# Kernel tuning notes

Measured on AMD Instinct MI355X. Metric: run time of the kernel, lower is better.

Reference implementation:

```python
import jax, jax.numpy as jnp
import numpy as np

D_MODEL, D_K, D_V, H = 1024, 64, 64, 16
B, NQ, NK = 2, 2048, 2048


def setup_inputs() -> dict:
    key = jax.random.key(0)
    ks = jax.random.split(key, 12)
    hd = H * D_K
    xav = lambda k, shape: jax.random.uniform(k, shape, jnp.float32, -1.0, 1.0) * np.sqrt(6.0 / (shape[0] + shape[1]))
    return {
        "queries": jax.random.normal(ks[0], (B, NQ, D_MODEL), jnp.float32),
        "keys": jax.random.normal(ks[1], (B, NK, D_MODEL), jnp.float32),
        "values": jax.random.normal(ks[2], (B, NK, D_MODEL), jnp.float32),
        "memory": jax.random.uniform(ks[3], (B, NK), jnp.float32),
        "Wq": xav(ks[4], (D_MODEL, hd)), "bq": jnp.zeros((hd,), jnp.float32),
        "Wk": xav(ks[5], (D_MODEL, hd)), "bk": jnp.zeros((hd,), jnp.float32),
        "Wv": xav(ks[6], (D_MODEL, H * D_V)), "bv": jnp.zeros((H * D_V,), jnp.float32),
        "Wo": xav(ks[7], (H * D_V, D_MODEL)), "bo": jnp.zeros((D_MODEL,), jnp.float32),
        "Wmm": xav(ks[8], (1, H * D_V)), "bmm": jnp.zeros((H * D_V,), jnp.float32),
    }


def reference(queries, keys, values, memory, Wq, bq, Wk, bk, Wv, bv, Wo, bo, Wmm, bmm):
    b, nq = queries.shape[:2]
    nk = keys.shape[1]
    # projections -> (b, h, n, d)
    q = (queries @ Wq + bq).reshape(b, nq, H, D_K).transpose(0, 2, 1, 3)
    k = (keys @ Wk + bk).reshape(b, nk, H, D_K).transpose(0, 2, 1, 3)
    v = (values @ Wv + bv).reshape(b, nk, H, D_V).transpose(0, 2, 1, 3)
    # memory gate: fc_mm(memory[..., None]) -> (b, nk, h*d_k) -> (b, h, nk, d_k)
    mm = (memory[:, :, None] * Wmm[0] + bmm).reshape(b, nk, H, D_K).transpose(0, 2, 1, 3)
    att = jnp.einsum("bhqd,bhkd->bhqk", q, k * mm) / np.sqrt(D_K).astype(np.float32)
    att = jax.nn.softmax(att, axis=-1)
    out = jnp.einsum("bhqk,bhkd->bhqd", att, v * mm)
    out = out.transpose(0, 2, 1, 3).reshape(b, nq, H * D_V)
    return out @ Wo + bo
```

## Files before the change

### kernel.cpp

```cpp
#include <hip/hip_runtime.h>
#include <hip/hip_bf16.h>

#define H_   16
#define NQ_  2048
#define NK_  2048
#define DM_  1024

typedef float f32x4 __attribute__((ext_vector_type(4)));
typedef __bf16 bf16x8 __attribute__((ext_vector_type(8)));
typedef unsigned short u16x8 __attribute__((ext_vector_type(8)));

__device__ __forceinline__ unsigned short bfbits(float x) {
  __bf16 h = (__bf16)x;
  return __builtin_bit_cast(unsigned short, h);
}

__global__ __launch_bounds__(256) void cvt3(const float* __restrict__ q,
                                            const float* __restrict__ k,
                                            const float* __restrict__ v,
                                            unsigned short* __restrict__ qo,
                                            unsigned short* __restrict__ ko,
                                            unsigned short* __restrict__ vo) {
  const float* src = (blockIdx.y == 0) ? q : (blockIdx.y == 1) ? k : v;
  unsigned short* dst = (blockIdx.y == 0) ? qo : (blockIdx.y == 1) ? ko : vo;
  int i = blockIdx.x * 256 + threadIdx.x;
  const float4* s4 = (const float4*)src;
  float4 a = s4[2 * i], b = s4[2 * i + 1];
  bf16x8 o;
  o[0] = (__bf16)a.x; o[1] = (__bf16)a.y; o[2] = (__bf16)a.z; o[3] = (__bf16)a.w;
  o[4] = (__bf16)b.x; o[5] = (__bf16)b.y; o[6] = (__bf16)b.z; o[7] = (__bf16)b.w;
  *((bf16x8*)dst + i) = o;
}

__global__ __launch_bounds__(256) void transpose_cvt4(
    const float* __restrict__ s0, const float* __restrict__ s1,
    const float* __restrict__ s2, const float* __restrict__ s3,
    unsigned short* __restrict__ d0, unsigned short* __restrict__ d1,
    unsigned short* __restrict__ d2, unsigned short* __restrict__ d3) {
  const float* src = (blockIdx.z == 0) ? s0 : (blockIdx.z == 1) ? s1 : (blockIdx.z == 2) ? s2 : s3;
  unsigned short* dst = (blockIdx.z == 0) ? d0 : (blockIdx.z == 1) ? d1 : (blockIdx.z == 2) ? d2 : d3;
  __shared__ float t[64][65];
  const int r0 = blockIdx.x * 64, c0 = blockIdx.y * 64;
  for (int i = threadIdx.x; i < 4096; i += 256) {
    int r = i >> 6, c = i & 63;
    t[r][c] = src[(size_t)(r0 + r) * DM_ + c0 + c];
  }
  __syncthreads();
  for (int i = threadIdx.x; i < 4096; i += 256) {
    int n = i >> 6, k = i & 63;
    dst[(size_t)(c0 + n) * DM_ + r0 + k] = bfbits(t[k][n]);
  }
}

__device__ __forceinline__ void gll16(const unsigned short* g, unsigned short* l) {
  __builtin_amdgcn_global_load_lds((const __attribute__((address_space(1))) void*)g,
                                   (__attribute__((address_space(3))) void*)l, 16, 0, 0);
}

template <int MODE>
__device__ __forceinline__ void gemm128_body(
    int bx, int by,
    const unsigned short* __restrict__ A, const unsigned short* __restrict__ Bt, int K,
    const float* __restrict__ bias, const float* __restrict__ mem,
    const float* __restrict__ Wmm, const float* __restrict__ bmm,
    unsigned short* __restrict__ obf,
    unsigned short* Al, unsigned short* Bl) {
  const int tid = threadIdx.x, lane = tid & 63, w = tid >> 6;
  const int wm = w >> 1, wn = w & 1;
  const int m0 = bx * 128, n0 = by * 128;
  const int lrow = lane >> 2, lcol = (lane & 3) * 8;
  const int fr = lane & 15, fk = (lane >> 4) * 8;

  f32x4 acc[4][4] = {};

  const unsigned short* ag0 = A + (size_t)(m0 + w * 32 + lrow) * K + lcol;
  const unsigned short* bg0 = Bt + (size_t)(n0 + w * 32 + lrow) * K + lcol;
  unsigned short* la0 = &Al[(w * 32) * 32];
  unsigned short* la1 = &Al[(w * 32 + 16) * 32];
  unsigned short* lb0 = &Bl[(w * 32) * 32];
  unsigned short* lb1 = &Bl[(w * 32 + 16) * 32];
  const size_t s16K = (size_t)16 * K;

  const int KT = K >> 5;
  for (int kt = 0; kt < KT; ++kt) {
    gll16(ag0, la0); gll16(ag0 + s16K, la1);
    gll16(bg0, lb0); gll16(bg0 + s16K, lb1);
    ag0 += 32; bg0 += 32;
    __syncthreads();
    bf16x8 af[4], bfr[4];
#pragma unroll
    for (int i = 0; i < 4; ++i) af[i] = *(const bf16x8*)&Al[(wm * 64 + i * 16 + fr) * 32 + fk];
#pragma unroll
    for (int j = 0; j < 4; ++j) bfr[j] = *(const bf16x8*)&Bl[(wn * 64 + j * 16 + fr) * 32 + fk];
#pragma unroll
    for (int i = 0; i < 4; ++i)
#pragma unroll
      for (int j = 0; j < 4; ++j)
        acc[i][j] = __builtin_amdgcn_mfma_f32_16x16x32_bf16(af[i], bfr[j], acc[i][j], 0, 0, 0);
    __syncthreads();
  }

#pragma unroll
  for (int i = 0; i < 4; ++i) {
    const int rowb = m0 + wm * 64 + i * 16 + (lane >> 4) * 4;
#pragma unroll
    for (int j = 0; j < 4; ++j) {
      const int col = n0 + wn * 64 + j * 16 + fr;
#pragma unroll
      for (int r = 0; r < 4; ++r) {
        float v = acc[i][j][r];
        int rr = rowb + r;
        if (MODE == 0) {
          int b = rr >> 11, nq = rr & 2047, h = col >> 6, d = col & 63;
          float val = (v + bias[col]) * 0.180336884f;
          obf[(((size_t)(b * H_ + h)) * NQ_ + nq) * 64 + d] = bfbits(val);
        } else if (MODE == 1) {
          int b = rr >> 11, nk = rr & 2047, h = col >> 6, d = col & 63;
          float gate = mem[b * NK_ + nk] * Wmm[col] + bmm[col];
          float val = (v + bias[col]) * gate;
          obf[(((size_t)(b * H_ + h)) * NK_ + nk) * 64 + d] = bfbits(val);
        } else {
          int b = col >> 11, key = col & 2047, h = rr >> 6, d = rr & 63;
          float gate = mem[b * NK_ + key] * Wmm[rr] + bmm[rr];
          float val = (v + bias[rr]) * gate;
          int keyp = (key & ~31) | ((key & 12) << 1) | ((key & 16) >> 2) | (key & 3);
          obf[(((size_t)(b * H_ + h)) * 64 + d) * NK_ + keyp] = bfbits(val);
        }
      }
    }
  }
}

__global__ __launch_bounds__(256) void gemm_qkv3(
    const unsigned short* __restrict__ qbf, const unsigned short* __restrict__ kbf,
    const unsigned short* __restrict__ vbf, const unsigned short* __restrict__ WvT,
    const unsigned short* __restrict__ WqT, const unsigned short* __restrict__ WkT,
    const float* __restrict__ bq, const float* __restrict__ bk, const float* __restrict__ bv,
    const float* __restrict__ mem, const float* __restrict__ Wmm, const float* __restrict__ bmm,
    unsigned short* __restrict__ Qp, unsigned short* __restrict__ Kp,
    unsigned short* __restrict__ VpT) {
  __shared__ unsigned short Al[128 * 32];
  __shared__ unsigned short Bl[128 * 32];
  const int gid = (blockIdx.x & 7) * 96 + (blockIdx.x >> 3);
  if (gid < 256) {
    gemm128_body<0>(gid & 31, gid >> 5, qbf, WqT, 1024, bq, nullptr, nullptr, nullptr,
                    Qp, Al, Bl);
  } else if (gid < 512) {
    int bb = gid - 256;
    gemm128_body<1>(bb & 31, bb >> 5, kbf, WkT, 1024, bk, mem, Wmm, bmm, Kp, Al, Bl);
  } else {
    int bb = gid - 512;
    gemm128_body<2>(bb & 7, bb >> 3, WvT, vbf, 1024, bv, mem, Wmm, bmm, VpT, Al, Bl);
  }
}

__global__ __launch_bounds__(256) void gemm_out(
    const unsigned short* __restrict__ AO, const unsigned short* __restrict__ WoT,
    const float* __restrict__ bo, float* __restrict__ out) {
  __shared__ unsigned short Al[64 * 32];
  __shared__ unsigned short Bl[128 * 32];
  const int b = (blockIdx.x & 7) * 64 + (blockIdx.x >> 3);
  const int bx = b & 63, by = b >> 6;
  const int tid = threadIdx.x, lane = tid & 63, w = tid >> 6;
  const int wm = w >> 1, wn = w & 1;
  const int m0 = bx * 64, n0 = by * 128;
  const int lrow = lane >> 2, lcol = (lane & 3) * 8;
  const int fr = lane & 15, fk = (lane >> 4) * 8;
  const int K = 1024;

  f32x4 acc[2][4] = {};

  const unsigned short* ag = AO + (size_t)(m0 + w * 16 + lrow) * K + lcol;
  const unsigned short* bg = WoT + (size_t)(n0 + w * 32 + lrow) * K + lcol;
  unsigned short* la0 = &Al[(w * 16) * 32];
  unsigned short* lb0 = &Bl[(w * 32) * 32];
  unsigned short* lb1 = &Bl[(w * 32 + 16) * 32];
  const size_t s16K = (size_t)16 * K;

  for (int kt = 0; kt < 32; ++kt) {
    gll16(ag, la0);
    gll16(bg, lb0); gll16(bg + s16K, lb1);
    ag += 32; bg += 32;
    __syncthreads();
    bf16x8 af[2], bfr[4];
#pragma unroll
    for (int i = 0; i < 2; ++i) af[i] = *(const bf16x8*)&Al[(wm * 32 + i * 16 + fr) * 32 + fk];
#pragma unroll
    for (int j = 0; j < 4; ++j) bfr[j] = *(const bf16x8*)&Bl[(wn * 64 + j * 16 + fr) * 32 + fk];
#pragma unroll
    for (int i = 0; i < 2; ++i)
#pragma unroll
      for (int j = 0; j < 4; ++j)
        acc[i][j] = __builtin_amdgcn_mfma_f32_16x16x32_bf16(af[i], bfr[j], acc[i][j], 0, 0, 0);
    __syncthreads();
  }

#pragma unroll
  for (int i = 0; i < 2; ++i) {
    const int rowb = m0 + wm * 32 + i * 16 + (lane >> 4) * 4;
#pragma unroll
    for (int j = 0; j < 4; ++j) {
      const int col = n0 + wn * 64 + j * 16 + fr;
#pragma unroll
      for (int r = 0; r < 4; ++r)
        out[(size_t)(rowb + r) * DM_ + col] = acc[i][j][r] + bo[col];
    }
  }
}

__global__ __launch_bounds__(512, 6) void flash_attn(const unsigned short* __restrict__ Qp,
                                                     const unsigned short* __restrict__ Kp,
                                                     const unsigned short* __restrict__ VpT,
                                                     unsigned short* __restrict__ AO) {
  __shared__ unsigned short Ks[2][64][72];
  __shared__ unsigned short Vs[2][64][72];

  const int tid = threadIdx.x, lane = tid & 63, w = tid >> 6;
  const int gid = (blockIdx.x & 7) * 64 + (blockIdx.x >> 3);
  const int bh = gid >> 4;
  const int qt = gid & 15;
  const int fr = lane & 15, hi = lane >> 4, fk8 = hi * 8;
  const int w16 = w * 16;

  const unsigned short* qg = Qp + (((size_t)bh * NQ_) + qt * 128 + w16 + fr) * 64;
  bf16x8 aq0 = *(const bf16x8*)&qg[fk8];
  bf16x8 aq1 = *(const bf16x8*)&qg[32 + fk8];

  const int srow = tid >> 3, scol = (tid & 7) * 8;
  const unsigned short* kg = Kp + ((size_t)bh * NK_ + srow) * 64 + scol;
  const unsigned short* vg = VpT + ((size_t)bh * 64 + srow) * NK_ + scol;

  f32x4 acc_o[4] = {};
  float m_run = -1e30f, l_run = 0.0f;

  {
    u16x8 k0 = *(const u16x8*)kg;
    u16x8 v0 = *(const u16x8*)vg;
    *(u16x8*)&Ks[0][srow][scol] = k0;
    *(u16x8*)&Vs[0][srow][scol] = v0;
  }

  u16x8 kreg, vreg;
  for (int kt = 0; kt < 32; ++kt) {
    const int cur = kt & 1;
    if (kt + 1 < 32) {
      kreg = *(const u16x8*)(kg + (kt + 1) * 64 * 64);
      vreg = *(const u16x8*)(vg + (kt + 1) * 64);
    }
    __syncthreads();

    f32x4 sv[4];
    __builtin_amdgcn_s_setprio(1);
#pragma unroll
    for (int kk = 0; kk < 4; ++kk) {
      bf16x8 b0 = *(const bf16x8*)&Ks[cur][kk * 16 + fr][fk8];
      bf16x8 b1 = *(const bf16x8*)&Ks[cur][kk * 16 + fr][32 + fk8];
      f32x4 z = {0.f, 0.f, 0.f, 0.f};
      z = __builtin_amdgcn_mfma_f32_16x16x32_bf16(b0, aq0, z, 0, 0, 0);
      sv[kk] = __builtin_amdgcn_mfma_f32_16x16x32_bf16(b1, aq1, z, 0, 0, 0);
    }
    __builtin_amdgcn_s_setprio(0);

    float mx = fmaxf(fmaxf(sv[0][0], sv[0][1]), fmaxf(sv[0][2], sv[0][3]));
#pragma unroll
    for (int kk = 1; kk < 4; ++kk)
      mx = fmaxf(mx, fmaxf(fmaxf(sv[kk][0], sv[kk][1]), fmaxf(sv[kk][2], sv[kk][3])));
    mx = fmaxf(mx, __shfl_xor(mx, 16));
    mx = fmaxf(mx, __shfl_xor(mx, 32));

    if (__any(mx > m_run + 8.0f)) {
      float mnew = fmaxf(m_run, mx);
      float sc = __builtin_amdgcn_exp2f(m_run - mnew);
      m_run = mnew;
      l_run *= sc;
#pragma unroll
      for (int r = 0; r < 4; ++r) {
        float scr = __shfl(sc, hi * 4 + r);
#pragma unroll
        for (int n = 0; n < 4; ++n) acc_o[n][r] *= scr;
      }
    }

    float ps = 0.0f;
    bf16x8 pa0, pa1;
#pragma unroll
    for (int kk = 0; kk < 4; ++kk) {
#pragma unroll
      for (int r = 0; r < 4; ++r) {
        float pv = __builtin_amdgcn_exp2f(sv[kk][r] - m_run);
        ps += pv;
        if (kk < 2) pa0[(kk & 1) * 4 + r] = (__bf16)pv;
        else        pa1[(kk & 1) * 4 + r] = (__bf16)pv;
      }
    }
    ps += __shfl_xor(ps, 16);
    ps += __shfl_xor(ps, 32);
    l_run += ps;

    __builtin_amdgcn_s_setprio(1);
#pragma unroll
    for (int ks = 0; ks < 2; ++ks) {
      bf16x8 pa = ks ? pa1 : pa0;
#pragma unroll
      for (int n = 0; n < 4; ++n) {
        bf16x8 vb = *(const bf16x8*)&Vs[cur][n * 16 + fr][ks * 32 + fk8];
        acc_o[n] = __builtin_amdgcn_mfma_f32_16x16x32_bf16(pa, vb, acc_o[n], 0, 0, 0);
      }
    }
    __builtin_amdgcn_s_setprio(0);

    if (kt + 1 < 32) {
      *(u16x8*)&Ks[cur ^ 1][srow][scol] = kreg;
      *(u16x8*)&Vs[cur ^ 1][srow][scol] = vreg;
    }
  }

  const int b = bh >> 4, h = bh & 15;
  float linv[4];
#pragma unroll
  for (int r = 0; r < 4; ++r) linv[r] = 1.0f / __shfl(l_run, hi * 4 + r);
#pragma unroll
  for (int n = 0; n < 4; ++n)
#pragma unroll
    for (int r = 0; r < 4; ++r) {
      float val = acc_o[n][r] * linv[r];
      int qrow = qt * 128 + w16 + hi * 4 + r;
      int col = h * 64 + n * 16 + fr;
      AO[(((size_t)b * NQ_ + qrow) << 10) + col] = bfbits(val);
    }
}

extern "C" void kernel_launch(void* const* d_in, const int* in_sizes, int n_in,
                              void* d_out, int out_size, void* d_ws, size_t ws_size,
                              hipStream_t stream) {
  const float* queries = (const float*)d_in[0];
  const float* keys    = (const float*)d_in[1];
  const float* values  = (const float*)d_in[2];
  const float* memory  = (const float*)d_in[3];
  const float* Wq  = (const float*)d_in[4];
  const float* bq  = (const float*)d_in[5];
  const float* Wk  = (const float*)d_in[6];
  const float* bk  = (const float*)d_in[7];
  const float* Wv  = (const float*)d_in[8];
  const float* bv  = (const float*)d_in[9];
  const float* Wo  = (const float*)d_in[10];
  const float* bo  = (const float*)d_in[11];
  const float* Wmm = (const float*)d_in[12];
  const float* bmm = (const float*)d_in[13];

  char* ws = (char*)d_ws;
  const size_t SZ_X = (size_t)4096 * 1024 * 2;
  const size_t SZ_W = (size_t)1024 * 1024 * 2;
  unsigned short* qbf = (unsigned short*)(ws);
  unsigned short* kbf = (unsigned short*)(ws + SZ_X);
  unsigned short* vbf = (unsigned short*)(ws + 2 * SZ_X);
  unsigned short* AO  = (unsigned short*)(ws);
  size_t off = 3 * SZ_X;
  unsigned short* WqT = (unsigned short*)(ws + off); off += SZ_W;
  unsigned short* WkT = (unsigned short*)(ws + off); off += SZ_W;
  unsigned short* WvT = (unsigned short*)(ws + off); off += SZ_W;
  unsigned short* WoT = (unsigned short*)(ws + off); off += SZ_W;
  unsigned short* Qp  = (unsigned short*)(ws + off); off += SZ_X;
  unsigned short* Kp  = (unsigned short*)(ws + off); off += SZ_X;
  unsigned short* VpT = (unsigned short*)(ws + off); off += SZ_X;

  cvt3<<<dim3(2048, 3), 256, 0, stream>>>(queries, keys, values, qbf, kbf, vbf);
  transpose_cvt4<<<dim3(16, 16, 4), 256, 0, stream>>>(Wq, Wk, Wv, Wo, WqT, WkT, WvT, WoT);

  gemm_qkv3<<<768, 256, 0, stream>>>(qbf, kbf, vbf, WvT, WqT, WkT,
                                     bq, bk, bv, memory, Wmm, bmm, Qp, Kp, VpT);

  flash_attn<<<512, 512, 0, stream>>>(Qp, Kp, VpT, AO);

  gemm_out<<<512, 256, 0, stream>>>(AO, WoT, bo, (float*)d_out);
}
```

Before: 144.3 us.

## Switch flash attention to 32x32x16 MFMA with 4 waves of 32 query rows

Rewrites the attention kernel to use 32x32x16 bf16 MFMA with the computed transposed (S^T = K·Q^T, O^T = V^T·P^T) so each lane owns one query row. Softmax max, sum and rescale then need no cross-row shuffles. Blocks shrink to 256 threads, each wave handling 32 query rows, and the V key permutation in the QKV projection is changed to match the new P fragment layout. The aim is fewer MFMA issues and less LDS and shuffle traffic, at the cost of larger accumulators (register pressure) and a tighter LDS padding (66) that may raise bank conflicts.

```diff
diff --git a/kernel.cpp b/kernel.cpp
--- a/kernel.cpp
+++ b/kernel.cpp
@@ -7,8 +7,10 @@
 #define DM_  1024
 
 typedef float f32x4 __attribute__((ext_vector_type(4)));
+typedef float f32x16 __attribute__((ext_vector_type(16)));
 typedef __bf16 bf16x8 __attribute__((ext_vector_type(8)));
 typedef unsigned short u16x8 __attribute__((ext_vector_type(8)));
+typedef unsigned short u16x4 __attribute__((ext_vector_type(4)));
 
 __device__ __forceinline__ unsigned short bfbits(float x) {
   __bf16 h = (__bf16)x;
@@ -123,7 +125,7 @@
           int b = col >> 11, key = col & 2047, h = rr >> 6, d = rr & 63;
           float gate = mem[b * NK_ + key] * Wmm[rr] + bmm[rr];
           float val = (v + bias[rr]) * gate;
-          int keyp = (key & ~31) | ((key & 12) << 1) | ((key & 16) >> 2) | (key & 3);
+          int keyp = (key & ~12) | ((key & 4) << 1) | ((key & 8) >> 1);
           obf[(((size_t)(b * H_ + h)) * 64 + d) * NK_ + keyp] = bfbits(val);
         }
       }
@@ -208,64 +210,65 @@
   }
 }
 
-__global__ __launch_bounds__(512, 6) void flash_attn(const unsigned short* __restrict__ Qp,
+__global__ __launch_bounds__(256, 2) void flash_attn(const unsigned short* __restrict__ Qp,
                                                      const unsigned short* __restrict__ Kp,
                                                      const unsigned short* __restrict__ VpT,
                                                      unsigned short* __restrict__ AO) {
-  __shared__ unsigned short Ks[2][64][72];
-  __shared__ unsigned short Vs[2][64][72];
+  __shared__ unsigned short Ks[2][64][66];
+  __shared__ unsigned short Vs[2][64][66];
 
   const int tid = threadIdx.x, lane = tid & 63, w = tid >> 6;
   const int gid = (blockIdx.x & 7) * 64 + (blockIdx.x >> 3);
   const int bh = gid >> 4;
   const int qt = gid & 15;
-  const int fr = lane & 15, hi = lane >> 4, fk8 = hi * 8;
-  const int w16 = w * 16;
-
-  const unsigned short* qg = Qp + (((size_t)bh * NQ_) + qt * 128 + w16 + fr) * 64;
-  bf16x8 aq0 = *(const bf16x8*)&qg[fk8];
-  bf16x8 aq1 = *(const bf16x8*)&qg[32 + fk8];
-
-  const int srow = tid >> 3, scol = (tid & 7) * 8;
+  const int r31 = lane & 31, hi2 = lane >> 5;
+
+  const unsigned short* qg = Qp + (((size_t)bh * NQ_) + qt * 128 + w * 32 + r31) * 64 + hi2 * 8;
+  bf16x8 qf0 = *(const bf16x8*)&qg[0];
+  bf16x8 qf1 = *(const bf16x8*)&qg[16];
+  bf16x8 qf2 = *(const bf16x8*)&qg[32];
+  bf16x8 qf3 = *(const bf16x8*)&qg[48];
+
+  const int srow = tid >> 2, scol = (tid & 3) * 16;
   const unsigned short* kg = Kp + ((size_t)bh * NK_ + srow) * 64 + scol;
   const unsigned short* vg = VpT + ((size_t)bh * 64 + srow) * NK_ + scol;
 
-  f32x4 acc_o[4] = {};
+  f32x16 acc0 = {}, acc1 = {};
   float m_run = -1e30f, l_run = 0.0f;
 
-  {
-    u16x8 k0 = *(const u16x8*)kg;
-    u16x8 v0 = *(const u16x8*)vg;
-    *(u16x8*)&Ks[0][srow][scol] = k0;
-    *(u16x8*)&Vs[0][srow][scol] = v0;
-  }
-
-  u16x8 kreg, vreg;
+  *(u16x8*)&Ks[0][srow][scol]     = *(const u16x8*)(kg);
+  *(u16x8*)&Ks[0][srow][scol + 8] = *(const u16x8*)(kg + 8);
+  *(u16x8*)&Vs[0][srow][scol]     = *(const u16x8*)(vg);
+  *(u16x8*)&Vs[0][srow][scol + 8] = *(const u16x8*)(vg + 8);
+
+  u16x8 kr0, kr1, vr0, vr1;
   for (int kt = 0; kt < 32; ++kt) {
     const int cur = kt & 1;
     if (kt + 1 < 32) {
-      kreg = *(const u16x8*)(kg + (kt + 1) * 64 * 64);
-      vreg = *(const u16x8*)(vg + (kt + 1) * 64);
-    }
-    __syncthreads();
-
-    f32x4 sv[4];
+      const unsigned short* kn = kg + (kt + 1) * 64 * 64;
+      const unsigned short* vn = vg + (kt + 1) * 64;
+      kr0 = *(const u16x8*)kn; kr1 = *(const u16x8*)(kn + 8);
+      vr0 = *(const u16x8*)vn; vr1 = *(const u16x8*)(vn + 8);
+    }
+    __syncthreads();
+
+    f32x16 sv0 = {}, sv1 = {};
     __builtin_amdgcn_s_setprio(1);
 #pragma unroll
-    for (int kk = 0; kk < 4; ++kk) {
-      bf16x8 b0 = *(const bf16x8*)&Ks[cur][kk * 16 + fr][fk8];
-      bf16x8 b1 = *(const bf16x8*)&Ks[cur][kk * 16 + fr][32 + fk8];
-      f32x4 z = {0.f, 0.f, 0.f, 0.f};
-      z = __builtin_amdgcn_mfma_f32_16x16x32_bf16(b0, aq0, z, 0, 0, 0);
-      sv[kk] = __builtin_amdgcn_mfma_f32_16x16x32_bf16(b1, aq1, z, 0, 0, 0);
+    for (int s = 0; s < 4; ++s) {
+      bf16x8 qf = (s == 0) ? qf0 : (s == 1) ? qf1 : (s == 2) ? qf2 : qf3;
+      bf16x8 ka0 = *(const bf16x8*)&Ks[cur][r31][s * 16 + hi2 * 8];
+      bf16x8 ka1 = *(const bf16x8*)&Ks[cur][32 + r31][s * 16 + hi2 * 8];
+      sv0 = __builtin_amdgcn_mfma_f32_32x32x16_bf16(ka0, qf, sv0, 0, 0, 0);
+      sv1 = __builtin_amdgcn_mfma_f32_32x32x16_bf16(ka1, qf, sv1, 0, 0, 0);
     }
     __builtin_amdgcn_s_setprio(0);
 
-    float mx = fmaxf(fmaxf(sv[0][0], sv[0][1]), fmaxf(sv[0][2], sv[0][3]));
-#pragma unroll
-    for (int kk = 1; kk < 4; ++kk)
-      mx = fmaxf(mx, fmaxf(fmaxf(sv[kk][0], sv[kk][1]), fmaxf(sv[kk][2], sv[kk][3])));
-    mx = fmaxf(mx, __shfl_xor(mx, 16));
+    float mx = fmaxf(sv0[0], sv0[1]);
+#pragma unroll
+    for (int g = 2; g < 16; ++g) mx = fmaxf(mx, sv0[g]);
+#pragma unroll
+    for (int g = 0; g < 16; ++g) mx = fmaxf(mx, sv1[g]);
     mx = fmaxf(mx, __shfl_xor(mx, 32));
 
     if (__any(mx > m_run + 8.0f)) {
@@ -273,61 +276,57 @@
       float sc = __builtin_amdgcn_exp2f(m_run - mnew);
       m_run = mnew;
       l_run *= sc;
-#pragma unroll
-      for (int r = 0; r < 4; ++r) {
-        float scr = __shfl(sc, hi * 4 + r);
-#pragma unroll
-        for (int n = 0; n < 4; ++n) acc_o[n][r] *= scr;
-      }
+      acc0 *= sc;
+      acc1 *= sc;
     }
 
     float ps = 0.0f;
-    bf16x8 pa0, pa1;
-#pragma unroll
-    for (int kk = 0; kk < 4; ++kk) {
-#pragma unroll
-      for (int r = 0; r < 4; ++r) {
-        float pv = __builtin_amdgcn_exp2f(sv[kk][r] - m_run);
-        ps += pv;
-        if (kk < 2) pa0[(kk & 1) * 4 + r] = (__bf16)pv;
-        else        pa1[(kk & 1) * 4 + r] = (__bf16)pv;
-      }
-    }
-    ps += __shfl_xor(ps, 16);
+    bf16x8 pb0, pb1, pb2, pb3;
+#pragma unroll
+    for (int g = 0; g < 16; ++g) {
+      float p0 = __builtin_amdgcn_exp2f(sv0[g] - m_run);
+      float p1 = __builtin_amdgcn_exp2f(sv1[g] - m_run);
+      ps += p0 + p1;
+      if (g < 8) { pb0[g] = (__bf16)p0; pb2[g] = (__bf16)p1; }
+      else       { pb1[g - 8] = (__bf16)p0; pb3[g - 8] = (__bf16)p1; }
+    }
     ps += __shfl_xor(ps, 32);
     l_run += ps;
 
     __builtin_amdgcn_s_setprio(1);
 #pragma unroll
-    for (int ks = 0; ks < 2; ++ks) {
-      bf16x8 pa = ks ? pa1 : pa0;
-#pragma unroll
-      for (int n = 0; n < 4; ++n) {
-        bf16x8 vb = *(const bf16x8*)&Vs[cur][n * 16 + fr][ks * 32 + fk8];
-        acc_o[n] = __builtin_amdgcn_mfma_f32_16x16x32_bf16(pa, vb, acc_o[n], 0, 0, 0);
-      }
+    for (int t = 0; t < 4; ++t) {
+      bf16x8 pb = (t == 0) ? pb0 : (t == 1) ? pb1 : (t == 2) ? pb2 : pb3;
+      bf16x8 va0 = *(const bf16x8*)&Vs[cur][r31][t * 16 + hi2 * 8];
+      bf16x8 va1 = *(const bf16x8*)&Vs[cur][32 + r31][t * 16 + hi2 * 8];
+      acc0 = __builtin_amdgcn_mfma_f32_32x32x16_bf16(va0, pb, acc0, 0, 0, 0);
+      acc1 = __builtin_amdgcn_mfma_f32_32x32x16_bf16(va1, pb, acc1, 0, 0, 0);
     }
     __builtin_amdgcn_s_setprio(0);
 
     if (kt + 1 < 32) {
-      *(u16x8*)&Ks[cur ^ 1][srow][scol] = kreg;
-      *(u16x8*)&Vs[cur ^ 1][srow][scol] = vreg;
+      *(u16x8*)&Ks[cur ^ 1][srow][scol]     = kr0;
+      *(u16x8*)&Ks[cur ^ 1][srow][scol + 8] = kr1;
+      *(u16x8*)&Vs[cur ^ 1][srow][scol]     = vr0;
+      *(u16x8*)&Vs[cur ^ 1][srow][scol + 8] = vr1;
     }
   }
 
   const int b = bh >> 4, h = bh & 15;
-  float linv[4];
-#pragma unroll
-  for (int r = 0; r < 4; ++r) linv[r] = 1.0f / __shfl(l_run, hi * 4 + r);
-#pragma unroll
-  for (int n = 0; n < 4; ++n)
-#pragma unroll
-    for (int r = 0; r < 4; ++r) {
-      float val = acc_o[n][r] * linv[r];
-      int qrow = qt * 128 + w16 + hi * 4 + r;
-      int col = h * 64 + n * 16 + fr;
-      AO[(((size_t)b * NQ_ + qrow) << 10) + col] = bfbits(val);
-    }
+  const float linv = 1.0f / l_run;
+  const int qrow = qt * 128 + w * 32 + r31;
+  const size_t rowbase = (((size_t)b * NQ_ + qrow) << 10) + h * 64;
+#pragma unroll
+  for (int c = 0; c < 4; ++c) {
+    u16x4 o0, o1;
+#pragma unroll
+    for (int i = 0; i < 4; ++i) {
+      o0[i] = bfbits(acc0[c * 4 + i] * linv);
+      o1[i] = bfbits(acc1[c * 4 + i] * linv);
+    }
+    *(u16x4*)&AO[rowbase + 8 * c + 4 * hi2]      = o0;
+    *(u16x4*)&AO[rowbase + 32 + 8 * c + 4 * hi2] = o1;
+  }
 }
 
 extern "C" void kernel_launch(void* const* d_in, const int* in_sizes, int n_in,
@@ -370,7 +369,7 @@
   gemm_qkv3<<<768, 256, 0, stream>>>(qbf, kbf, vbf, WvT, WqT, WkT,
                                      bq, bk, bv, memory, Wmm, bmm, Qp, Kp, VpT);
 
-  flash_attn<<<512, 512, 0, stream>>>(Qp, Kp, VpT, AO);
+  flash_attn<<<512, 256, 0, stream>>>(Qp, Kp, VpT, AO);
 
   gemm_out<<<512, 256, 0, stream>>>(AO, WoT, bo, (float*)d_out);
 }
```

After: 138.1 us. -4.3%, faster.
